# Kernel tuning notes

Measured on AMD Instinct MI355X. Metric: run time of the kernel, lower is better.

Reference implementation:

```python
import jax, jax.numpy as jnp
import numpy as np

THRESHOLD = 0.5
NEG_POS = 3
ALPHA = 1.0


def cxcy_to_xy(c):
    return jnp.concatenate([c[..., :2] - c[..., 2:] / 2, c[..., :2] + c[..., 2:] / 2], axis=-1)


def xy_to_cxcy(x):
    return jnp.concatenate([(x[..., :2] + x[..., 2:]) / 2, x[..., 2:] - x[..., :2]], axis=-1)


def encode_gcxgcy(cxcy, priors_cxcy):
    # SSD offset encoding with variances (10, 10, 5, 5)
    return jnp.concatenate([
        (cxcy[..., :2] - priors_cxcy[..., :2]) / (priors_cxcy[..., 2:] / 10.0),
        jnp.log(cxcy[..., 2:] / priors_cxcy[..., 2:]) * 5.0,
    ], axis=-1)


def compute_iou(a, b):
    # a: [n,4] xyxy, b: [m,4] xyxy -> [n,m]
    lt = jnp.maximum(a[:, None, :2], b[None, :, :2])
    rb = jnp.minimum(a[:, None, 2:], b[None, :, 2:])
    wh = jnp.clip(rb - lt, 0.0)
    inter = wh[..., 0] * wh[..., 1]
    area_a = (a[:, 2] - a[:, 0]) * (a[:, 3] - a[:, 1])
    area_b = (b[:, 2] - b[:, 0]) * (b[:, 3] - b[:, 1])
    return inter / (area_a[:, None] + area_b[None, :] - inter)


def _match_one(boxes, labels, db_xy, db_cxcy):
    # boxes: [n_obj,4] xyxy, labels: [n_obj], priors: [P,4]
    n_obj = boxes.shape[0]
    overlaps = compute_iou(boxes, db_xy)                 # [n_obj, P]
    ov_per_box = jnp.max(overlaps, axis=0)               # [P]
    obj_per_box = jnp.argmax(overlaps, axis=0)           # [P]
    box_per_obj = jnp.argmax(overlaps, axis=1)           # [n_obj]
    # force each gt to own its best prior
    obj_per_box = obj_per_box.at[box_per_obj].set(jnp.arange(n_obj))
    ov_per_box = ov_per_box.at[box_per_obj].set(1.0)
    lbl = labels[obj_per_box]                            # [P]
    lbl = jnp.where(ov_per_box < THRESHOLD, 0, lbl)      # background below threshold
    true_locs = encode_gcxgcy(xy_to_cxcy(boxes[obj_per_box]), db_cxcy)  # [P,4]
    return true_locs, lbl


def smooth_l1(x):
    ax = jnp.abs(x)
    return jnp.where(ax < 1.0, 0.5 * x * x, ax - 0.5)


def reference(loc_pred, cls_pred, gt_boxes, gt_labels, default_boxes):
    # loc_pred: [B,P,4], cls_pred: [B,P,C], gt_boxes: [B,n_obj,4],
    # gt_labels: [B,n_obj] int, default_boxes: [P,4] cxcywh
    db_xy = cxcy_to_xy(default_boxes)
    true_locs, true_labels = jax.vmap(_match_one, in_axes=(0, 0, None, None))(
        gt_boxes, gt_labels, db_xy, default_boxes)      # [B,P,4], [B,P]

    positive = true_labels > 0                           # [B,P]
    n_pos = jnp.sum(positive, axis=1)                    # [B]
    n_pos_total = jnp.sum(n_pos).astype(loc_pred.dtype)

    # localization loss: SmoothL1 mean over positive box elements
    loc_elem = smooth_l1(loc_pred - true_locs)           # [B,P,4]
    loc_loss = jnp.sum(loc_elem * positive[..., None]) / (n_pos_total * 4.0)

    # confidence loss: cross entropy with 3:1 hard negative mining
    logp = jax.nn.log_softmax(cls_pred, axis=-1)         # [B,P,C]
    ce = -jnp.take_along_axis(logp, true_labels[..., None], axis=-1)[..., 0]  # [B,P]
    conf_pos = jnp.sum(ce * positive)
    ce_neg = jnp.where(positive, 0.0, ce)
    # rank negatives by loss (descending) per image; take top neg_pos * n_pos
    ranks = jnp.argsort(jnp.argsort(-ce_neg, axis=1), axis=1)  # [B,P]
    hard_neg = ranks < (NEG_POS * n_pos)[:, None]
    conf_hard = jnp.sum(ce_neg * hard_neg)
    conf_loss = (conf_pos + conf_hard) / n_pos_total

    return conf_loss + ALPHA * loc_loss


def setup_inputs() -> dict:
    key = jax.random.key(0)
    ks = jax.random.split(key, 8)
    B, P, C, n_obj = 64, 8732, 81, 32

    # priors in cxcywh, valid in [0,1]
    db_cxy = jax.random.uniform(ks[0], (P, 2), minval=0.05, maxval=0.95)
    db_wh = jax.random.uniform(ks[1], (P, 2), minval=0.05, maxval=0.3)
    default_boxes = jnp.concatenate([db_cxy, db_wh], axis=-1).astype(jnp.float32)

    # gt boxes: valid xyxy built from centers and sizes
    g_cxy = jax.random.uniform(ks[2], (B, n_obj, 2), minval=0.2, maxval=0.8)
    g_wh = jax.random.uniform(ks[3], (B, n_obj, 2), minval=0.1, maxval=0.4)
    gt_boxes = jnp.concatenate([g_cxy - g_wh / 2, g_cxy + g_wh / 2], axis=-1).astype(jnp.float32)
    gt_labels = jax.random.randint(ks[4], (B, n_obj), 1, C)

    loc_pred = jax.random.normal(ks[5], (B, P, 4), dtype=jnp.float32) * 0.1
    cls_pred = jax.random.normal(ks[6], (B, P, C), dtype=jnp.float32)

    return {"loc_pred": loc_pred, "cls_pred": cls_pred, "gt_boxes": gt_boxes,
            "gt_labels": gt_labels, "default_boxes": default_boxes}
```

## Files before the change

kernel.cpp:

```cpp
#include <hip/hip_runtime.h>
#include <hip/hip_bf16.h>
#include <math.h>

#define BB 64
#define PP 8732
#define CC 81
#define NOBJ 32
#define CHUNKS ((PP + 255) / 256)
#define NPRI (BB * PP)
#define WTILE 16
#define WTW (WTILE * CC)
#define NWT (NPRI / WTILE)
#define CE_BLOCKS 1792

typedef float f4 __attribute__((ext_vector_type(4)));

__device__ __forceinline__ float sl1(float x) {
    float ax = fabsf(x);
    return (ax < 1.0f) ? 0.5f * x * x : ax - 0.5f;
}

__global__ __launch_bounds__(256) void k_bestprior(
    const float* __restrict__ gt_boxes,
    const float* __restrict__ dbox,
    int* __restrict__ bp)
{
    const int wave = threadIdx.x >> 6, lane = threadIdx.x & 63;
    const int b = blockIdx.x >> 3;
    const int o = ((blockIdx.x & 7) << 2) + wave;

    const float* g = gt_boxes + (b * NOBJ + o) * 4;
    float gx0 = g[0], gy0 = g[1], gx1 = g[2], gy1 = g[3];
    float garea = (gx1 - gx0) * (gy1 - gy0);

    float best = -1.0f; int bpp = 0x7fffffff;
    for (int p = lane; p < PP; p += 64) {
        float4 db = reinterpret_cast<const float4*>(dbox)[p];
        float px0 = db.x - db.z * 0.5f, py0 = db.y - db.w * 0.5f;
        float px1 = db.x + db.z * 0.5f, py1 = db.y + db.w * 0.5f;
        float parea = db.z * db.w;
        float lx = fmaxf(px0, gx0), ly = fmaxf(py0, gy0);
        float rx = fminf(px1, gx1), ry = fminf(py1, gy1);
        float w = fmaxf(rx - lx, 0.0f), h = fmaxf(ry - ly, 0.0f);
        float inter = w * h;
        float iou = inter / (garea + parea - inter);
        if (iou > best) { best = iou; bpp = p; }
    }
#pragma unroll
    for (int m = 32; m > 0; m >>= 1) {
        float ov = __shfl_xor(best, m);
        int   op = __shfl_xor(bpp, m);
        if (ov > best || (ov == best && op < bpp)) { best = ov; bpp = op; }
    }
    if (lane == 0) bp[b * NOBJ + o] = bpp;
}

__global__ __launch_bounds__(256) void k_assign(
    const float* __restrict__ loc_pred,
    const float* __restrict__ gt_boxes,
    const int*   __restrict__ gt_labels,
    const float* __restrict__ dbox,
    const int*   __restrict__ bp,
    int*   __restrict__ true_label,
    int*   __restrict__ n_pos,
    float* __restrict__ acc,
    int*   __restrict__ n_pos_total)
{
    __shared__ float s_gx0[NOBJ], s_gy0[NOBJ], s_gx1[NOBJ], s_gy1[NOBJ], s_garea[NOBJ];
    __shared__ float s_gcx[NOBJ], s_gcy[NOBJ], s_gw[NOBJ], s_gh[NOBJ];
    __shared__ int   s_glbl[NOBJ], s_bp[NOBJ];
    __shared__ float red_f[256];
    __shared__ int   red_i[256];

    const int b     = blockIdx.x / CHUNKS;
    const int chunk = blockIdx.x % CHUNKS;
    const int tid   = threadIdx.x;
    const int p     = chunk * 256 + tid;

    if (tid < NOBJ) {
        float x0 = gt_boxes[(b * NOBJ + tid) * 4 + 0];
        float y0 = gt_boxes[(b * NOBJ + tid) * 4 + 1];
        float x1 = gt_boxes[(b * NOBJ + tid) * 4 + 2];
        float y1 = gt_boxes[(b * NOBJ + tid) * 4 + 3];
        s_gx0[tid] = x0; s_gy0[tid] = y0; s_gx1[tid] = x1; s_gy1[tid] = y1;
        s_garea[tid] = (x1 - x0) * (y1 - y0);
        s_gcx[tid] = (x0 + x1) * 0.5f;
        s_gcy[tid] = (y0 + y1) * 0.5f;
        s_gw[tid]  = x1 - x0;
        s_gh[tid]  = y1 - y0;
        s_glbl[tid] = gt_labels[b * NOBJ + tid];
        s_bp[tid]   = bp[b * NOBJ + tid];
    }
    __syncthreads();

    float loc_local = 0.0f;
    int   np_local  = 0;

    if (p < PP) {
        float4 db = reinterpret_cast<const float4*>(dbox)[p];
        float px0 = db.x - db.z * 0.5f, py0 = db.y - db.w * 0.5f;
        float px1 = db.x + db.z * 0.5f, py1 = db.y + db.w * 0.5f;
        float parea = db.z * db.w;

        float best = -1.0f; int bo = 0;
#pragma unroll
        for (int o = 0; o < NOBJ; ++o) {
            float lx = fmaxf(px0, s_gx0[o]), ly = fmaxf(py0, s_gy0[o]);
            float rx = fminf(px1, s_gx1[o]), ry = fminf(py1, s_gy1[o]);
            float w = fmaxf(rx - lx, 0.0f), h = fmaxf(ry - ly, 0.0f);
            float inter = w * h;
            float iou = inter / (s_garea[o] + parea - inter);
            if (iou > best) { best = iou; bo = o; }
        }
        int forced = -1;
#pragma unroll
        for (int o = 0; o < NOBJ; ++o)
            if (s_bp[o] == p) forced = o;

        int o_use, lbl;
        if (forced >= 0) { o_use = forced; lbl = s_glbl[forced]; }
        else             { o_use = bo; lbl = (best < 0.5f) ? 0 : s_glbl[bo]; }

        true_label[b * PP + p] = lbl;
        if (lbl > 0) {
            np_local = 1;
            float g0 = (s_gcx[o_use] - db.x) / (db.z / 10.0f);
            float g1 = (s_gcy[o_use] - db.y) / (db.w / 10.0f);
            float g2 = logf(s_gw[o_use] / db.z) * 5.0f;
            float g3 = logf(s_gh[o_use] / db.w) * 5.0f;
            float4 lp = reinterpret_cast<const float4*>(loc_pred)[b * PP + p];
            loc_local = sl1(lp.x - g0) + sl1(lp.y - g1) + sl1(lp.z - g2) + sl1(lp.w - g3);
        }
    }

    red_f[tid] = loc_local;
    red_i[tid] = np_local;
    __syncthreads();
#pragma unroll
    for (int st = 128; st > 0; st >>= 1) {
        if (tid < st) { red_f[tid] += red_f[tid + st]; red_i[tid] += red_i[tid + st]; }
        __syncthreads();
    }
    if (tid == 0) {
        atomicAdd(&acc[0], red_f[0]);
        atomicAdd(&n_pos[b], red_i[0]);
        atomicAdd(n_pos_total, red_i[0]);
    }
}

__global__ __launch_bounds__(256) void k_ce(
    const float* __restrict__ cls_pred,
    const int*   __restrict__ true_label,
    float* __restrict__ ce_neg,
    float* __restrict__ acc)
{
    __shared__ float s_x[4][WTW];
    __shared__ float s_red[4];
    const int tid  = threadIdx.x;
    const int wave = tid >> 6, lane = tid & 63;
    const int rloc = lane >> 2, q = lane & 3;
    const int NW   = CE_BLOCKS * 4;

    float* sx = s_x[wave];
    f4* dst = reinterpret_cast<f4*>(sx);

    const float L2E = 1.4426950408889634f;
    const float LN2 = 0.6931471805599453f;
    float local = 0.0f;

    int wt = blockIdx.x * 4 + wave;
    f4 r0, r1, r2, r3, r4, r5;
    int lbl_next = 0;
    if (wt < NWT) {
        const f4* src = reinterpret_cast<const f4*>(cls_pred + (size_t)wt * WTW);
        r0 = __builtin_nontemporal_load(src + lane);
        r1 = __builtin_nontemporal_load(src + 64 + lane);
        r2 = __builtin_nontemporal_load(src + 128 + lane);
        r3 = __builtin_nontemporal_load(src + 192 + lane);
        r4 = __builtin_nontemporal_load(src + 256 + lane);
        if (lane < 4) r5 = __builtin_nontemporal_load(src + 320 + lane);
        lbl_next = true_label[wt * WTILE + rloc];
    }

    while (wt < NWT) {
        dst[lane] = r0; dst[64 + lane] = r1; dst[128 + lane] = r2;
        dst[192 + lane] = r3; dst[256 + lane] = r4;
        if (lane < 4) dst[320 + lane] = r5;
        const int lbl  = lbl_next;
        const int pidx = wt * WTILE + rloc;

        wt += NW;
        if (wt < NWT) {
            const f4* src = reinterpret_cast<const f4*>(cls_pred + (size_t)wt * WTW);
            r0 = __builtin_nontemporal_load(src + lane);
            r1 = __builtin_nontemporal_load(src + 64 + lane);
            r2 = __builtin_nontemporal_load(src + 128 + lane);
            r3 = __builtin_nontemporal_load(src + 192 + lane);
            r4 = __builtin_nontemporal_load(src + 256 + lane);
            if (lane < 4) r5 = __builtin_nontemporal_load(src + 320 + lane);
            lbl_next = true_label[wt * WTILE + rloc];
        }

        const float* x = sx + rloc * CC;
        const int base = q * 20;
        float s0 = 0.0f, s1 = 0.0f;
#pragma unroll
        for (int j = 0; j < 20; j += 2) {
            s0 += exp2f(x[base + j]     * L2E);
            s1 += exp2f(x[base + j + 1] * L2E);
        }
        float s = s0 + s1;
        if (q == 3) s += exp2f(x[80] * L2E);
        s += __shfl_xor(s, 1);
        s += __shfl_xor(s, 2);

        if (q == 0) {
            float ce = fmaf(log2f(s), LN2, -x[lbl]);
            ce_neg[pidx] = (lbl > 0) ? 0.0f : ce;
            local += (lbl > 0) ? ce : 0.0f;
        }
    }

#pragma unroll
    for (int m = 32; m > 0; m >>= 1) local += __shfl_xor(local, m);
    if (lane == 0) s_red[wave] = local;
    __syncthreads();
    if (tid == 0) {
        float tot = s_red[0] + s_red[1] + s_red[2] + s_red[3];
        if (tot != 0.0f) atomicAdd(&acc[1], tot);
    }
}

__global__ __launch_bounds__(1024) void k_select(
    const float* __restrict__ ce_neg,
    const int*   __restrict__ n_pos,
    float* __restrict__ acc,
    const int*  __restrict__ n_pos_total,
    int*   __restrict__ done,
    float* __restrict__ out)
{
    __shared__ unsigned int sv[PP];
    __shared__ unsigned int hist[257];
    __shared__ unsigned int wtot[4];
    __shared__ unsigned int s_prefix, s_krem;
    __shared__ float red_f[1024];
    __shared__ int   red_i[1024];

    const int b = blockIdx.x, tid = threadIdx.x, lane = tid & 63;

    int K = n_pos[b] * 3;
    if (K > PP) K = PP;

    if (K > 0) {
        for (int i = tid; i < PP; i += 1024)
            sv[i] = __float_as_uint(ce_neg[b * PP + i]);
        __syncthreads();

        unsigned int prefix = 0, krem = (unsigned int)K;
        for (int shift = 24; shift >= 0; shift -= 8) {
            if (tid < 256) hist[tid] = 0;
            if (tid == 0) hist[256] = 0;
            __syncthreads();
            unsigned int mask_hi = (shift == 24) ? 0u : (0xFFFFFFFFu << (shift + 8));
            for (int i = tid; i < PP; i += 1024) {
                unsigned int v = sv[i];
                if ((v & mask_hi) == prefix) atomicAdd(&hist[(v >> shift) & 0xFFu], 1u);
            }
            __syncthreads();
            unsigned int s = 0;
            if (tid < 256) {
                s = hist[tid];
#pragma unroll
                for (int off = 1; off < 64; off <<= 1) {
                    unsigned int a = __shfl_down(s, off);
                    if (lane + off < 64) s += a;
                }
                if (lane == 0) wtot[tid >> 6] = s;
            }
            __syncthreads();
            if (tid < 256) {
                for (int w2 = (tid >> 6) + 1; w2 < 4; ++w2) s += wtot[w2];
                hist[tid] = s;
            }
            __syncthreads();
            if (tid < 256) {
                unsigned int suf  = hist[tid];
                unsigned int suf1 = hist[tid + 1];
                if (suf >= krem && suf1 < krem) {
                    s_prefix = prefix | ((unsigned int)tid << shift);
                    s_krem   = krem - suf1;
                }
            }
            __syncthreads();
            prefix = s_prefix; krem = s_krem;
        }
        float cutoff = __uint_as_float(prefix);

        float sum_gt = 0.0f; int cnt_gt = 0;
        for (int i = tid; i < PP; i += 1024) {
            float v = __uint_as_float(sv[i]);
            if (v > cutoff) { sum_gt += v; cnt_gt++; }
        }
        red_f[tid] = sum_gt; red_i[tid] = cnt_gt;
        __syncthreads();
#pragma unroll
        for (int st = 512; st > 0; st >>= 1) {
            if (tid < st) { red_f[tid] += red_f[tid + st]; red_i[tid] += red_i[tid + st]; }
            __syncthreads();
        }
        if (tid == 0)
            atomicAdd(&acc[2], red_f[0] + (float)(K - red_i[0]) * cutoff);
    }

    if (tid == 0) {
        __threadfence();
        int old = atomicAdd(done, 1);
        if (old == BB - 1) {
            float a0 = atomicAdd(&acc[0], 0.0f);
            float a1 = atomicAdd(&acc[1], 0.0f);
            float a2 = atomicAdd(&acc[2], 0.0f);
            float npt = (float)atomicAdd((int*)n_pos_total, 0);
            out[0] = (a1 + a2) / npt + a0 / (npt * 4.0f);
        }
    }
}

extern "C" void kernel_launch(void* const* d_in, const int* in_sizes, int n_in,
                              void* d_out, int out_size, void* d_ws, size_t ws_size,
                              hipStream_t stream) {
    const float* loc_pred  = (const float*)d_in[0];
    const float* cls_pred  = (const float*)d_in[1];
    const float* gt_boxes  = (const float*)d_in[2];
    const int*   gt_labels = (const int*)d_in[3];
    const float* dbox      = (const float*)d_in[4];
    float* out = (float*)d_out;

    float* acc        = (float*)d_ws;
    int*   npt        = (int*)d_ws + 3;
    int*   done       = (int*)d_ws + 4;
    int*   n_pos      = (int*)d_ws + 8;
    int*   bp         = (int*)d_ws + 8 + BB;
    int*   true_label = (int*)d_ws + 8 + BB + BB * NOBJ;
    float* ce_neg     = (float*)((int*)d_ws + 8 + BB + BB * NOBJ + (size_t)NPRI);

    hipMemsetAsync(d_ws, 0, 32, stream);
    hipMemsetAsync(n_pos, 0, BB * sizeof(int), stream);

    k_bestprior<<<BB * (NOBJ / 4), 256, 0, stream>>>(gt_boxes, dbox, bp);
    k_assign<<<BB * CHUNKS, 256, 0, stream>>>(loc_pred, gt_boxes, gt_labels, dbox, bp,
                                              true_label, n_pos, acc, npt);
    k_ce<<<CE_BLOCKS, 256, 0, stream>>>(cls_pred, true_label, ce_neg, acc);
    k_select<<<BB, 1024, 0, stream>>>(ce_neg, n_pos, acc, npt, done, out);
}
```

Baseline: 167.6 us.

## Fuse best-prior and label-independent log-sum-exp into one pre-kernel, gather CE in select

The log-sum-exp over classes does not depend on the matched labels, so it is now computed in the same launch as the best-prior IoU search, using extra blocks. This removes the serial dependency of the CE pass on k_assign. The per-prior cross-entropy is finished inside k_select by gathering the label logit from cls_pred, and the positive-CE sum is reduced there too. The two memsets are replaced by zeroing inside block 0 of the pre-kernel, which cuts launch count at the cost of a scattered gather of logits in the select kernel.

```diff
diff --git a/kernel.cpp b/kernel.cpp
--- a/kernel.cpp
+++ b/kernel.cpp
@@ -11,7 +11,9 @@
 #define WTILE 16
 #define WTW (WTILE * CC)
 #define NWT (NPRI / WTILE)
-#define CE_BLOCKS 1792
+#define LSE_BLOCKS 1792
+#define BP_BLOCKS (BB * (NOBJ / 4))
+#define PRE_BLOCKS (BP_BLOCKS + LSE_BLOCKS)
 
 typedef float f4 __attribute__((ext_vector_type(4)));
 
@@ -20,39 +22,111 @@
     return (ax < 1.0f) ? 0.5f * x * x : ax - 0.5f;
 }
 
-__global__ __launch_bounds__(256) void k_bestprior(
+__global__ __launch_bounds__(256) void k_pre(
     const float* __restrict__ gt_boxes,
     const float* __restrict__ dbox,
-    int* __restrict__ bp)
+    const float* __restrict__ cls_pred,
+    int*   __restrict__ bp,
+    float* __restrict__ lse,
+    float* __restrict__ acc,
+    int*   __restrict__ npt,
+    int*   __restrict__ done,
+    int*   __restrict__ n_pos)
 {
-    const int wave = threadIdx.x >> 6, lane = threadIdx.x & 63;
-    const int b = blockIdx.x >> 3;
-    const int o = ((blockIdx.x & 7) << 2) + wave;
-
-    const float* g = gt_boxes + (b * NOBJ + o) * 4;
-    float gx0 = g[0], gy0 = g[1], gx1 = g[2], gy1 = g[3];
-    float garea = (gx1 - gx0) * (gy1 - gy0);
-
-    float best = -1.0f; int bpp = 0x7fffffff;
-    for (int p = lane; p < PP; p += 64) {
-        float4 db = reinterpret_cast<const float4*>(dbox)[p];
-        float px0 = db.x - db.z * 0.5f, py0 = db.y - db.w * 0.5f;
-        float px1 = db.x + db.z * 0.5f, py1 = db.y + db.w * 0.5f;
-        float parea = db.z * db.w;
-        float lx = fmaxf(px0, gx0), ly = fmaxf(py0, gy0);
-        float rx = fminf(px1, gx1), ry = fminf(py1, gy1);
-        float w = fmaxf(rx - lx, 0.0f), h = fmaxf(ry - ly, 0.0f);
-        float inter = w * h;
-        float iou = inter / (garea + parea - inter);
-        if (iou > best) { best = iou; bpp = p; }
-    }
-#pragma unroll
-    for (int m = 32; m > 0; m >>= 1) {
-        float ov = __shfl_xor(best, m);
-        int   op = __shfl_xor(bpp, m);
-        if (ov > best || (ov == best && op < bpp)) { best = ov; bpp = op; }
-    }
-    if (lane == 0) bp[b * NOBJ + o] = bpp;
+    __shared__ float s_x[4][WTW];
+    const int tid  = threadIdx.x;
+    const int wave = tid >> 6, lane = tid & 63;
+
+    if (blockIdx.x == 0) {
+        if (tid < BB) n_pos[tid] = 0;
+        else if (tid < BB + 3) acc[tid - BB] = 0.0f;
+        else if (tid == BB + 3) *npt = 0;
+        else if (tid == BB + 4) *done = 0;
+    }
+
+    if (blockIdx.x < BP_BLOCKS) {
+        const int b = blockIdx.x >> 3;
+        const int o = ((blockIdx.x & 7) << 2) + wave;
+
+        const float* g = gt_boxes + (b * NOBJ + o) * 4;
+        float gx0 = g[0], gy0 = g[1], gx1 = g[2], gy1 = g[3];
+        float garea = (gx1 - gx0) * (gy1 - gy0);
+
+        float best = -1.0f; int bpp = 0x7fffffff;
+        for (int p = lane; p < PP; p += 64) {
+            float4 db = reinterpret_cast<const float4*>(dbox)[p];
+            float px0 = db.x - db.z * 0.5f, py0 = db.y - db.w * 0.5f;
+            float px1 = db.x + db.z * 0.5f, py1 = db.y + db.w * 0.5f;
+            float parea = db.z * db.w;
+            float lx = fmaxf(px0, gx0), ly = fmaxf(py0, gy0);
+            float rx = fminf(px1, gx1), ry = fminf(py1, gy1);
+            float w = fmaxf(rx - lx, 0.0f), h = fmaxf(ry - ly, 0.0f);
+            float inter = w * h;
+            float iou = inter / (garea + parea - inter);
+            if (iou > best) { best = iou; bpp = p; }
+        }
+#pragma unroll
+        for (int m = 32; m > 0; m >>= 1) {
+            float ov = __shfl_xor(best, m);
+            int   op = __shfl_xor(bpp, m);
+            if (ov > best || (ov == best && op < bpp)) { best = ov; bpp = op; }
+        }
+        if (lane == 0) bp[b * NOBJ + o] = bpp;
+        return;
+    }
+
+    const int rloc = lane >> 2, q = lane & 3;
+    const int NW   = LSE_BLOCKS * 4;
+    float* sx = s_x[wave];
+    f4* dst = reinterpret_cast<f4*>(sx);
+
+    const float L2E = 1.4426950408889634f;
+    const float LN2 = 0.6931471805599453f;
+
+    int wt = (blockIdx.x - BP_BLOCKS) * 4 + wave;
+    f4 r0, r1, r2, r3, r4, r5;
+    if (wt < NWT) {
+        const f4* src = reinterpret_cast<const f4*>(cls_pred + (size_t)wt * WTW);
+        r0 = __builtin_nontemporal_load(src + lane);
+        r1 = __builtin_nontemporal_load(src + 64 + lane);
+        r2 = __builtin_nontemporal_load(src + 128 + lane);
+        r3 = __builtin_nontemporal_load(src + 192 + lane);
+        r4 = __builtin_nontemporal_load(src + 256 + lane);
+        if (lane < 4) r5 = __builtin_nontemporal_load(src + 320 + lane);
+    }
+
+    while (wt < NWT) {
+        dst[lane] = r0; dst[64 + lane] = r1; dst[128 + lane] = r2;
+        dst[192 + lane] = r3; dst[256 + lane] = r4;
+        if (lane < 4) dst[320 + lane] = r5;
+        const int pidx = wt * WTILE + rloc;
+
+        wt += NW;
+        if (wt < NWT) {
+            const f4* src = reinterpret_cast<const f4*>(cls_pred + (size_t)wt * WTW);
+            r0 = __builtin_nontemporal_load(src + lane);
+            r1 = __builtin_nontemporal_load(src + 64 + lane);
+            r2 = __builtin_nontemporal_load(src + 128 + lane);
+            r3 = __builtin_nontemporal_load(src + 192 + lane);
+            r4 = __builtin_nontemporal_load(src + 256 + lane);
+            if (lane < 4) r5 = __builtin_nontemporal_load(src + 320 + lane);
+        }
+
+        const float* x = sx + rloc * CC;
+        const int base = q * 20;
+        float s0 = 0.0f, s1 = 0.0f;
+#pragma unroll
+        for (int j = 0; j < 20; j += 2) {
+            s0 += exp2f(x[base + j]     * L2E);
+            s1 += exp2f(x[base + j + 1] * L2E);
+        }
+        float s = s0 + s1;
+        if (q == 3) s += exp2f(x[80] * L2E);
+        s += __shfl_xor(s, 1);
+        s += __shfl_xor(s, 2);
+
+        if (q == 0) lse[pidx] = log2f(s) * LN2;
+    }
 }
 
 __global__ __launch_bounds__(256) void k_assign(
@@ -148,91 +222,10 @@
     }
 }
 
-__global__ __launch_bounds__(256) void k_ce(
+__global__ __launch_bounds__(1024) void k_select(
     const float* __restrict__ cls_pred,
+    const float* __restrict__ lse,
     const int*   __restrict__ true_label,
-    float* __restrict__ ce_neg,
-    float* __restrict__ acc)
-{
-    __shared__ float s_x[4][WTW];
-    __shared__ float s_red[4];
-    const int tid  = threadIdx.x;
-    const int wave = tid >> 6, lane = tid & 63;
-    const int rloc = lane >> 2, q = lane & 3;
-    const int NW   = CE_BLOCKS * 4;
-
-    float* sx = s_x[wave];
-    f4* dst = reinterpret_cast<f4*>(sx);
-
-    const float L2E = 1.4426950408889634f;
-    const float LN2 = 0.6931471805599453f;
-    float local = 0.0f;
-
-    int wt = blockIdx.x * 4 + wave;
-    f4 r0, r1, r2, r3, r4, r5;
-    int lbl_next = 0;
-    if (wt < NWT) {
-        const f4* src = reinterpret_cast<const f4*>(cls_pred + (size_t)wt * WTW);
-        r0 = __builtin_nontemporal_load(src + lane);
-        r1 = __builtin_nontemporal_load(src + 64 + lane);
-        r2 = __builtin_nontemporal_load(src + 128 + lane);
-        r3 = __builtin_nontemporal_load(src + 192 + lane);
-        r4 = __builtin_nontemporal_load(src + 256 + lane);
-        if (lane < 4) r5 = __builtin_nontemporal_load(src + 320 + lane);
-        lbl_next = true_label[wt * WTILE + rloc];
-    }
-
-    while (wt < NWT) {
-        dst[lane] = r0; dst[64 + lane] = r1; dst[128 + lane] = r2;
-        dst[192 + lane] = r3; dst[256 + lane] = r4;
-        if (lane < 4) dst[320 + lane] = r5;
-        const int lbl  = lbl_next;
-        const int pidx = wt * WTILE + rloc;
-
-        wt += NW;
-        if (wt < NWT) {
-            const f4* src = reinterpret_cast<const f4*>(cls_pred + (size_t)wt * WTW);
-            r0 = __builtin_nontemporal_load(src + lane);
-            r1 = __builtin_nontemporal_load(src + 64 + lane);
-            r2 = __builtin_nontemporal_load(src + 128 + lane);
-            r3 = __builtin_nontemporal_load(src + 192 + lane);
-            r4 = __builtin_nontemporal_load(src + 256 + lane);
-            if (lane < 4) r5 = __builtin_nontemporal_load(src + 320 + lane);
-            lbl_next = true_label[wt * WTILE + rloc];
-        }
-
-        const float* x = sx + rloc * CC;
-        const int base = q * 20;
-        float s0 = 0.0f, s1 = 0.0f;
-#pragma unroll
-        for (int j = 0; j < 20; j += 2) {
-            s0 += exp2f(x[base + j]     * L2E);
-            s1 += exp2f(x[base + j + 1] * L2E);
-        }
-        float s = s0 + s1;
-        if (q == 3) s += exp2f(x[80] * L2E);
-        s += __shfl_xor(s, 1);
-        s += __shfl_xor(s, 2);
-
-        if (q == 0) {
-            float ce = fmaf(log2f(s), LN2, -x[lbl]);
-            ce_neg[pidx] = (lbl > 0) ? 0.0f : ce;
-            local += (lbl > 0) ? ce : 0.0f;
-        }
-    }
-
-#pragma unroll
-    for (int m = 32; m > 0; m >>= 1) local += __shfl_xor(local, m);
-    if (lane == 0) s_red[wave] = local;
-    __syncthreads();
-    if (tid == 0) {
-        float tot = s_red[0] + s_red[1] + s_red[2] + s_red[3];
-        if (tot != 0.0f) atomicAdd(&acc[1], tot);
-    }
-}
-
-__global__ __launch_bounds__(1024) void k_select(
-    const float* __restrict__ ce_neg,
     const int*   __restrict__ n_pos,
     float* __restrict__ acc,
     const int*  __restrict__ n_pos_total,
@@ -248,14 +241,30 @@
 
     const int b = blockIdx.x, tid = threadIdx.x, lane = tid & 63;
 
+    float pos_local = 0.0f;
+    for (int i = tid; i < PP; i += 1024) {
+        const int idx = b * PP + i;
+        float l = lse[idx];
+        int lbl = true_label[idx];
+        float xl = cls_pred[(size_t)idx * CC + lbl];
+        float ce = fmaxf(l - xl, 0.0f);
+        if (lbl > 0) { pos_local += ce; sv[i] = 0u; }
+        else sv[i] = __float_as_uint(ce);
+    }
+    red_f[tid] = pos_local;
+    __syncthreads();
+#pragma unroll
+    for (int st = 512; st > 0; st >>= 1) {
+        if (tid < st) red_f[tid] += red_f[tid + st];
+        __syncthreads();
+    }
+    if (tid == 0 && red_f[0] != 0.0f) atomicAdd(&acc[1], red_f[0]);
+    __syncthreads();
+
     int K = n_pos[b] * 3;
     if (K > PP) K = PP;
 
     if (K > 0) {
-        for (int i = tid; i < PP; i += 1024)
-            sv[i] = __float_as_uint(ce_neg[b * PP + i]);
-        __syncthreads();
-
         unsigned int prefix = 0, krem = (unsigned int)K;
         for (int shift = 24; shift >= 0; shift -= 8) {
             if (tid < 256) hist[tid] = 0;
@@ -341,14 +350,12 @@
     int*   n_pos      = (int*)d_ws + 8;
     int*   bp         = (int*)d_ws + 8 + BB;
     int*   true_label = (int*)d_ws + 8 + BB + BB * NOBJ;
-    float* ce_neg     = (float*)((int*)d_ws + 8 + BB + BB * NOBJ + (size_t)NPRI);
-
-    hipMemsetAsync(d_ws, 0, 32, stream);
-    hipMemsetAsync(n_pos, 0, BB * sizeof(int), stream);
-
-    k_bestprior<<<BB * (NOBJ / 4), 256, 0, stream>>>(gt_boxes, dbox, bp);
+    float* lse        = (float*)((int*)d_ws + 8 + BB + BB * NOBJ + (size_t)NPRI);
+
+    k_pre<<<PRE_BLOCKS, 256, 0, stream>>>(gt_boxes, dbox, cls_pred,
+                                          bp, lse, acc, npt, done, n_pos);
     k_assign<<<BB * CHUNKS, 256, 0, stream>>>(loc_pred, gt_boxes, gt_labels, dbox, bp,
                                               true_label, n_pos, acc, npt);
-    k_ce<<<CE_BLOCKS, 256, 0, stream>>>(cls_pred, true_label, ce_neg, acc);
-    k_select<<<BB, 1024, 0, stream>>>(ce_neg, n_pos, acc, npt, done, out);
-}
+    k_select<<<BB, 1024, 0, stream>>>(cls_pred, lse, true_label, n_pos,
+                                      acc, npt, done, out);
+}
```

Result: slower. 177.2 us (+5.7%).

## Fold workspace zeroing into bestprior, widen bestprior blocks, privatize select histograms

Applied to the files above, without the earlier changes.

Drops the two memset launches by having block 0 of the best-prior kernel zero the accumulators and per-image positive counts. Each best-prior block now handles one object with all 256 threads and a cross-wave reduction, giving four times as many blocks. The radix-select kernel uses per-wave private histograms to cut LDS atomic contention, and warp-shuffle reductions replace the tree reductions. Atomics in the assign kernel are skipped when the contribution is zero. The zeroing now depends on kernel ordering in the stream rather than separate memsets.

```diff
diff --git a/kernel.cpp b/kernel.cpp
--- a/kernel.cpp
+++ b/kernel.cpp
@@ -23,18 +23,31 @@
 __global__ __launch_bounds__(256) void k_bestprior(
     const float* __restrict__ gt_boxes,
     const float* __restrict__ dbox,
-    int* __restrict__ bp)
+    int*   __restrict__ bp,
+    float* __restrict__ acc,
+    int*   __restrict__ npt,
+    int*   __restrict__ done,
+    int*   __restrict__ n_pos)
 {
-    const int wave = threadIdx.x >> 6, lane = threadIdx.x & 63;
-    const int b = blockIdx.x >> 3;
-    const int o = ((blockIdx.x & 7) << 2) + wave;
+    __shared__ float s_bv[4];
+    __shared__ int   s_bi[4];
+    const int tid = threadIdx.x, lane = tid & 63, wave = tid >> 6;
+    const int b = blockIdx.x >> 5;
+    const int o = blockIdx.x & 31;
+
+    if (blockIdx.x == 0) {
+        if (tid < BB) n_pos[tid] = 0;
+        else if (tid < BB + 3) acc[tid - BB] = 0.0f;
+        else if (tid == BB + 3) *npt = 0;
+        else if (tid == BB + 4) *done = 0;
+    }
 
     const float* g = gt_boxes + (b * NOBJ + o) * 4;
     float gx0 = g[0], gy0 = g[1], gx1 = g[2], gy1 = g[3];
     float garea = (gx1 - gx0) * (gy1 - gy0);
 
     float best = -1.0f; int bpp = 0x7fffffff;
-    for (int p = lane; p < PP; p += 64) {
+    for (int p = tid; p < PP; p += 256) {
         float4 db = reinterpret_cast<const float4*>(dbox)[p];
         float px0 = db.x - db.z * 0.5f, py0 = db.y - db.w * 0.5f;
         float px1 = db.x + db.z * 0.5f, py1 = db.y + db.w * 0.5f;
@@ -52,7 +65,16 @@
         int   op = __shfl_xor(bpp, m);
         if (ov > best || (ov == best && op < bpp)) { best = ov; bpp = op; }
     }
-    if (lane == 0) bp[b * NOBJ + o] = bpp;
+    if (lane == 0) { s_bv[wave] = best; s_bi[wave] = bpp; }
+    __syncthreads();
+    if (tid == 0) {
+        for (int w2 = 1; w2 < 4; ++w2) {
+            if (s_bv[w2] > best || (s_bv[w2] == best && s_bi[w2] < bpp)) {
+                best = s_bv[w2]; bpp = s_bi[w2];
+            }
+        }
+        bp[b * NOBJ + o] = bpp;
+    }
 }
 
 __global__ __launch_bounds__(256) void k_assign(
@@ -142,9 +164,11 @@
         __syncthreads();
     }
     if (tid == 0) {
-        atomicAdd(&acc[0], red_f[0]);
-        atomicAdd(&n_pos[b], red_i[0]);
-        atomicAdd(n_pos_total, red_i[0]);
+        if (red_f[0] != 0.0f) atomicAdd(&acc[0], red_f[0]);
+        if (red_i[0]) {
+            atomicAdd(&n_pos[b], red_i[0]);
+            atomicAdd(n_pos_total, red_i[0]);
+        }
     }
 }
 
@@ -240,13 +264,15 @@
     float* __restrict__ out)
 {
     __shared__ unsigned int sv[PP];
+    __shared__ unsigned int h16[16][256];
     __shared__ unsigned int hist[257];
     __shared__ unsigned int wtot[4];
     __shared__ unsigned int s_prefix, s_krem;
-    __shared__ float red_f[1024];
-    __shared__ int   red_i[1024];
-
-    const int b = blockIdx.x, tid = threadIdx.x, lane = tid & 63;
+    __shared__ float rf[16];
+    __shared__ int   ri[16];
+
+    const int b = blockIdx.x, tid = threadIdx.x;
+    const int lane = tid & 63, w = tid >> 6;
 
     int K = n_pos[b] * 3;
     if (K > PP) K = PP;
@@ -254,33 +280,44 @@
     if (K > 0) {
         for (int i = tid; i < PP; i += 1024)
             sv[i] = __float_as_uint(ce_neg[b * PP + i]);
-        __syncthreads();
 
         unsigned int prefix = 0, krem = (unsigned int)K;
         for (int shift = 24; shift >= 0; shift -= 8) {
-            if (tid < 256) hist[tid] = 0;
+            unsigned int* hflat = &h16[0][0];
+            for (int j = tid; j < 16 * 256; j += 1024) hflat[j] = 0;
             if (tid == 0) hist[256] = 0;
             __syncthreads();
             unsigned int mask_hi = (shift == 24) ? 0u : (0xFFFFFFFFu << (shift + 8));
             for (int i = tid; i < PP; i += 1024) {
                 unsigned int v = sv[i];
-                if ((v & mask_hi) == prefix) atomicAdd(&hist[(v >> shift) & 0xFFu], 1u);
+                if ((v & mask_hi) == prefix)
+                    atomicAdd(&h16[w][(v >> shift) & 0xFFu], 1u);
             }
             __syncthreads();
             unsigned int s = 0;
             if (tid < 256) {
-                s = hist[tid];
+#pragma unroll
+                for (int r = 0; r < 16; ++r) s += h16[r][tid];
 #pragma unroll
                 for (int off = 1; off < 64; off <<= 1) {
                     unsigned int a = __shfl_down(s, off);
                     if (lane + off < 64) s += a;
                 }
-                if (lane == 0) wtot[tid >> 6] = s;
+                if (lane == 0) wtot[w] = s;
             }
             __syncthreads();
             if (tid < 256) {
-                for (int w2 = (tid >> 6) + 1; w2 < 4; ++w2) s += wtot[w2];
-                hist[tid] = s;
+                unsigned int sb = 0;
+#pragma unroll
+                for (int r = 0; r < 16; ++r) sb += h16[r][tid];
+                unsigned int suf = sb;
+#pragma unroll
+                for (int off = 1; off < 64; off <<= 1) {
+                    unsigned int a = __shfl_down(suf, off);
+                    if (lane + off < 64) suf += a;
+                }
+                for (int w2 = w + 1; w2 < 4; ++w2) suf += wtot[w2];
+                hist[tid] = suf;
             }
             __syncthreads();
             if (tid < 256) {
@@ -301,15 +338,19 @@
             float v = __uint_as_float(sv[i]);
             if (v > cutoff) { sum_gt += v; cnt_gt++; }
         }
-        red_f[tid] = sum_gt; red_i[tid] = cnt_gt;
+#pragma unroll
+        for (int m = 32; m > 0; m >>= 1) {
+            sum_gt += __shfl_xor(sum_gt, m);
+            cnt_gt += __shfl_xor(cnt_gt, m);
+        }
+        if (lane == 0) { rf[w] = sum_gt; ri[w] = cnt_gt; }
         __syncthreads();
-#pragma unroll
-        for (int st = 512; st > 0; st >>= 1) {
-            if (tid < st) { red_f[tid] += red_f[tid + st]; red_i[tid] += red_i[tid + st]; }
-            __syncthreads();
-        }
-        if (tid == 0)
-            atomicAdd(&acc[2], red_f[0] + (float)(K - red_i[0]) * cutoff);
+        if (tid == 0) {
+            float sg = 0.0f; int cg = 0;
+#pragma unroll
+            for (int r = 0; r < 16; ++r) { sg += rf[r]; cg += ri[r]; }
+            atomicAdd(&acc[2], sg + (float)(K - cg) * cutoff);
+        }
     }
 
     if (tid == 0) {
@@ -341,12 +382,10 @@
     int*   n_pos      = (int*)d_ws + 8;
     int*   bp         = (int*)d_ws + 8 + BB;
     int*   true_label = (int*)d_ws + 8 + BB + BB * NOBJ;
-    float* ce_neg     = (float*)((int*)d_ws + 8 + BB + BB * NOBJ + (size_t)NPRI);
-
-    hipMemsetAsync(d_ws, 0, 32, stream);
-    hipMemsetAsync(n_pos, 0, BB * sizeof(int), stream);
-
-    k_bestprior<<<BB * (NOBJ / 4), 256, 0, stream>>>(gt_boxes, dbox, bp);
+    float* ce_neg     = (float*)(true_label + (size_t)NPRI);
+
+    k_bestprior<<<BB * NOBJ, 256, 0, stream>>>(gt_boxes, dbox, bp,
+                                               acc, npt, done, n_pos);
     k_assign<<<BB * CHUNKS, 256, 0, stream>>>(loc_pred, gt_boxes, gt_labels, dbox, bp,
                                               true_label, n_pos, acc, npt);
     k_ce<<<CE_BLOCKS, 256, 0, stream>>>(cls_pred, true_label, ce_neg, acc);
```

Result: faster. 150.6 us (-10.2%).
